# Performance work log

Measured on AMD Instinct MI355X. Metric: run time of the kernel, lower is better.

Reference implementation:

```python
import jax, jax.numpy as jnp
import numpy as np

CHUNK_SIZE = 1024  # module default chunk_size


def setup_inputs() -> dict:
    key = jax.random.key(0)
    kq, kk, kv = jax.random.split(key, 3)
    B, H, S, D = 2, 16, 2048, 64
    q = jax.random.normal(kq, (B, H, S, D), dtype=jnp.float32)
    k = jax.random.normal(kk, (B, H, S, D), dtype=jnp.float32)
    v = jax.random.normal(kv, (B, H, S, D), dtype=jnp.float32)
    return {"q": q, "k": k, "v": v}


def reference(q, k, v):
    # Chunked causal attention: q split into chunks of CHUNK_SIZE along seq,
    # each chunk attends to the full K/V with causal mask (tril, diagonal=start).
    B, H, S, D = q.shape
    scale = D ** (-0.5)
    cs = CHUNK_SIZE
    nc = S // cs  # S is a multiple of chunk_size here
    qc = q.reshape(B, H, nc, cs, D)
    # scores: [B, H, nc, cs, S]
    scores = jnp.einsum('bhncd,bhsd->bhncs', qc, k) * scale
    # causal mask per chunk: key position j visible iff j <= chunk_start + i
    row = (jnp.arange(nc) * cs)[:, None, None] + jnp.arange(cs)[None, :, None]  # [nc, cs, 1]
    col = jnp.arange(S)[None, None, :]  # [1, 1, S]
    causal = col <= row  # [nc, cs, S]
    scores = jnp.where(causal[None, None], scores, -jnp.inf)
    attn = jax.nn.softmax(scores, axis=-1)
    out = jnp.einsum('bhncs,bhsd->bhncd', attn, v)
    return out.reshape(B, H, S, D)
```

## Files before the change

kernel.cpp:

```cpp
#include <hip/hip_runtime.h>

typedef __bf16 bf16x8 __attribute__((ext_vector_type(8)));
typedef float f32x4 __attribute__((ext_vector_type(4)));

#define S_LEN 2048
#define D_DIM 64
#define NHEAD 32

typedef __attribute__((address_space(1))) const void gas;
typedef __attribute__((address_space(3))) void las;

__global__ __launch_bounds__(256) void convert_kv(const float* __restrict__ K,
                                                  const float* __restrict__ V,
                                                  __bf16* __restrict__ Kb,
                                                  __bf16* __restrict__ Vtg) {
    const int head = blockIdx.y;
    const int s0   = blockIdx.x * 64;
    const int tr   = threadIdx.x >> 2;
    const int tc   = (threadIdx.x & 3) << 4;
    const size_t ib = (size_t)head * (S_LEN * D_DIM) + (size_t)(s0 + tr) * D_DIM + tc;

    __shared__ __bf16 tb[64][72];

    {
        const float* kr = K + ib;
        f32x4 a = *(const f32x4*)kr, b = *(const f32x4*)(kr + 4),
              c = *(const f32x4*)(kr + 8), d = *(const f32x4*)(kr + 12);
        bf16x8 o0, o1;
        #pragma unroll
        for (int e = 0; e < 4; ++e) {
            o0[e] = (__bf16)a[e]; o0[e + 4] = (__bf16)b[e];
            o1[e] = (__bf16)c[e]; o1[e + 4] = (__bf16)d[e];
        }
        __bf16* ko = Kb + ib;
        *(bf16x8*)ko = o0; *(bf16x8*)(ko + 8) = o1;
    }
    {
        const float* vr = V + ib;
        f32x4 a = *(const f32x4*)vr, b = *(const f32x4*)(vr + 4),
              c = *(const f32x4*)(vr + 8), d = *(const f32x4*)(vr + 12);
        #pragma unroll
        for (int e = 0; e < 4; ++e) {
            tb[tc +  e][tr] = (__bf16)a[e];
            tb[tc + 4 + e][tr] = (__bf16)b[e];
            tb[tc + 8 + e][tr] = (__bf16)c[e];
            tb[tc + 12 + e][tr] = (__bf16)d[e];
        }
    }
    __syncthreads();
    {
        bf16x8 o0, o1;
        #pragma unroll
        for (int e = 0; e < 8; ++e) { o0[e] = tb[tr][tc + e]; o1[e] = tb[tr][tc + 8 + e]; }
        __bf16* vo = Vtg + (size_t)head * (D_DIM * S_LEN) + (size_t)tr * S_LEN + s0 + tc;
        *(bf16x8*)vo = o0; *(bf16x8*)(vo + 8) = o1;
    }
}

__global__ __launch_bounds__(256, 4) void attn_fwd(const float* __restrict__ Q,
                                                   const __bf16* __restrict__ Kb,
                                                   const __bf16* __restrict__ Vg,
                                                   float* __restrict__ O) {
    const int b    = blockIdx.x;
    const int xcd  = b & 7;
    const int cs   = (b >> 3) & 31;
    const int j    = b >> 8;
    const int head = xcd * 4 + (cs >> 3);
    const int slot = cs & 7;
    const int chunk = (j == 0) ? slot : (j == 1) ? (31 - slot)
                    : (j == 2) ? (slot + 8) : (23 - slot);

    const int tid  = threadIdx.x;
    const int wave = tid >> 6;
    const int lane = tid & 63;
    const int l15  = lane & 15;
    const int lhi  = lane >> 4;

    const int q0 = chunk * 64 + wave * 16;
    const size_t qbase = (size_t)head * (S_LEN * D_DIM);
    const size_t vbase = (size_t)head * (D_DIM * S_LEN);
    const float qscale = 0.125f * 1.44269504088896340736f;

    __shared__ __align__(16) __bf16 Klds[2][64][64];
    __shared__ __align__(16) __bf16 Vt[2][64][64];
    __shared__ __align__(16) __bf16 Plds[4][16][64];

    const int xsw = (lane & 7) ^ ((lane >> 3) & 7);
    const size_t kOff = (size_t)(lane >> 3) * D_DIM + (size_t)xsw * 8;
    const size_t vOff = (size_t)(lane >> 3) * S_LEN + (size_t)xsw * 8;
    const __bf16* kgw = Kb + qbase + (size_t)(wave * 16) * D_DIM + kOff;
    const __bf16* vgw = Vg + vbase + (size_t)(wave * 16) * S_LEN + vOff;

    bf16x8 qf[2];
    {
        const float* qrow = Q + qbase + (size_t)(q0 + l15) * D_DIM + lhi * 8;
        #pragma unroll
        for (int h = 0; h < 2; ++h) {
            f32x4 a = *(const f32x4*)(qrow + h * 32);
            f32x4 bq = *(const f32x4*)(qrow + h * 32 + 4);
            bf16x8 t;
            #pragma unroll
            for (int e = 0; e < 4; ++e) { t[e] = (__bf16)(a[e] * qscale); t[e + 4] = (__bf16)(bq[e] * qscale); }
            qf[h] = t;
        }
    }

    f32x4 acc[4];
    #pragma unroll
    for (int td = 0; td < 4; ++td) acc[td] = (f32x4){0.f, 0.f, 0.f, 0.f};
    float m_r = -1e30f, l_r = 0.f;

    auto stage = [&](int kv0, int bufi) {
        const __bf16* kg = kgw + (size_t)kv0 * D_DIM;
        const __bf16* vg = vgw + kv0;
        __builtin_amdgcn_global_load_lds((gas*)kg,                 (las*)&Klds[bufi][wave * 16][0],     16, 0, 0);
        __builtin_amdgcn_global_load_lds((gas*)(kg + 8 * D_DIM),   (las*)&Klds[bufi][wave * 16 + 8][0], 16, 0, 0);
        __builtin_amdgcn_global_load_lds((gas*)vg,                 (las*)&Vt[bufi][wave * 16][0],       16, 0, 0);
        __builtin_amdgcn_global_load_lds((gas*)(vg + 8 * S_LEN),   (las*)&Vt[bufi][wave * 16 + 8][0],   16, 0, 0);
    };

    stage(0, 0);

    const int nt = chunk + 1;
    for (int kt = 0; kt < nt; ++kt) {
        const int cur = kt & 1;
        asm volatile("s_waitcnt vmcnt(0)" ::: "memory");
        __syncthreads();

        if (kt + 1 < nt) stage((kt + 1) << 6, cur ^ 1);

        f32x4 s[4];
        #pragma unroll
        for (int ct = 0; ct < 4; ++ct) s[ct] = (f32x4){0.f, 0.f, 0.f, 0.f};
        __builtin_amdgcn_s_setprio(1);
        #pragma unroll
        for (int h = 0; h < 2; ++h) {
            #pragma unroll
            for (int ct = 0; ct < 4; ++ct) {
                const int krow = ct * 16 + l15;
                bf16x8 kf = *(const bf16x8*)&Klds[cur][krow][(h * 32 + lhi * 8) ^ ((l15 & 7) << 3)];
                s[ct] = __builtin_amdgcn_mfma_f32_16x16x32_bf16(kf, qf[h], s[ct], 0, 0, 0);
            }
        }
        __builtin_amdgcn_s_setprio(0);

        if (kt == nt - 1) {
            const int kv0 = kt << 6;
            const int qg = q0 + l15;
            #pragma unroll
            for (int ct = 0; ct < 4; ++ct)
                #pragma unroll
                for (int r = 0; r < 4; ++r) {
                    const int kg = kv0 + ct * 16 + lhi * 4 + r;
                    if (kg > qg) s[ct][r] = -1e30f;
                }
        }

        float mm = fmaxf(fmaxf(fmaxf(s[0][0], s[0][1]), fmaxf(s[0][2], s[0][3])),
                         fmaxf(fmaxf(s[1][0], s[1][1]), fmaxf(s[1][2], s[1][3])));
        mm = fmaxf(mm, fmaxf(fmaxf(fmaxf(s[2][0], s[2][1]), fmaxf(s[2][2], s[2][3])),
                             fmaxf(fmaxf(s[3][0], s[3][1]), fmaxf(s[3][2], s[3][3]))));
        mm = fmaxf(mm, __shfl_xor(mm, 16));
        mm = fmaxf(mm, __shfl_xor(mm, 32));
        if (!__all(mm - m_r <= 8.0f)) {
            const float mn = fmaxf(m_r, mm);
            const float f = exp2f(m_r - mn);
            m_r = mn;
            l_r *= f;
            #pragma unroll
            for (int r = 0; r < 4; ++r) {
                const float fr = __shfl(f, lhi * 4 + r);
                #pragma unroll
                for (int td = 0; td < 4; ++td) acc[td][r] *= fr;
            }
        }
        float ps = 0.f;
        #pragma unroll
        for (int ct = 0; ct < 4; ++ct)
            #pragma unroll
            for (int r = 0; r < 4; ++r) {
                const float p = exp2f(s[ct][r] - m_r);
                s[ct][r] = p;
                ps += p;
            }
        ps += __shfl_xor(ps, 16);
        ps += __shfl_xor(ps, 32);
        l_r += ps;

        #pragma unroll
        for (int ct = 0; ct < 4; ++ct) {
            union { __bf16 h[4]; unsigned long long u; } pw;
            #pragma unroll
            for (int r = 0; r < 4; ++r) pw.h[r] = (__bf16)s[ct][r];
            *(unsigned long long*)&Plds[wave][l15][(ct * 16 + lhi * 4) ^ ((l15 & 7) << 3)] = pw.u;
        }
        asm volatile("s_waitcnt lgkmcnt(0)" ::: "memory");
        bf16x8 pf[2];
        #pragma unroll
        for (int kh = 0; kh < 2; ++kh)
            pf[kh] = *(const bf16x8*)&Plds[wave][l15][(kh * 32 + lhi * 8) ^ ((l15 & 7) << 3)];
        asm volatile("" ::: "memory");

        __builtin_amdgcn_s_setprio(1);
        #pragma unroll
        for (int kh = 0; kh < 2; ++kh) {
            #pragma unroll
            for (int td = 0; td < 4; ++td) {
                const int vrow = td * 16 + l15;
                bf16x8 vf = *(const bf16x8*)&Vt[cur][vrow][(kh * 32 + lhi * 8) ^ ((vrow & 7) << 3)];
                acc[td] = __builtin_amdgcn_mfma_f32_16x16x32_bf16(pf[kh], vf, acc[td], 0, 0, 0);
            }
        }
        __builtin_amdgcn_s_setprio(0);
    }

    float* orow = O + qbase + (size_t)q0 * D_DIM;
    #pragma unroll
    for (int r = 0; r < 4; ++r) {
        const float inv = 1.0f / __shfl(l_r, lhi * 4 + r);
        #pragma unroll
        for (int td = 0; td < 4; ++td)
            orow[(size_t)(lhi * 4 + r) * D_DIM + td * 16 + l15] = acc[td][r] * inv;
    }
}

__global__ __launch_bounds__(256, 4) void attn_fwd_fb(const float* __restrict__ Q,
                                                      const float* __restrict__ K,
                                                      const float* __restrict__ V,
                                                      float* __restrict__ O) {
    const int b    = blockIdx.x;
    const int xcd  = b & 7;
    const int cs   = (b >> 3) & 31;
    const int j    = b >> 8;
    const int head = xcd * 4 + (cs >> 3);
    const int slot = cs & 7;
    const int chunk = (j == 0) ? slot : (j == 1) ? (31 - slot)
                    : (j == 2) ? (slot + 8) : (23 - slot);

    const int tid  = threadIdx.x;
    const int wave = tid >> 6;
    const int lane = tid & 63;
    const int l15  = lane & 15;
    const int lhi  = lane >> 4;

    const int q0 = chunk * 64 + wave * 16;
    const size_t base = (size_t)head * (S_LEN * D_DIM);
    const float qscale = 0.125f * 1.44269504088896340736f;

    __shared__ __align__(16) __bf16 Klds[2][64][64];
    __shared__ __align__(16) __bf16 Vt[2][64][64];
    __shared__ __align__(16) __bf16 Plds[4][16][64];

    const int rk = tid >> 2;
    const int ck = (tid & 3) << 4;
    const int kp = tid & 31;
    const int dc = tid >> 5;
    const int swk = (rk & 7) << 3;

    bf16x8 qf[2];
    {
        const float* qrow = Q + base + (size_t)(q0 + l15) * D_DIM + lhi * 8;
        #pragma unroll
        for (int h = 0; h < 2; ++h) {
            f32x4 a = *(const f32x4*)(qrow + h * 32);
            f32x4 bq = *(const f32x4*)(qrow + h * 32 + 4);
            bf16x8 t;
            #pragma unroll
            for (int e = 0; e < 4; ++e) { t[e] = (__bf16)(a[e] * qscale); t[e + 4] = (__bf16)(bq[e] * qscale); }
            qf[h] = t;
        }
    }

    f32x4 acc[4];
    #pragma unroll
    for (int td = 0; td < 4; ++td) acc[td] = (f32x4){0.f, 0.f, 0.f, 0.f};
    float m_r = -1e30f, l_r = 0.f;

    f32x4 pk[4], pva[2], pvb[2];
    {
        const float* ks = K + base + (size_t)rk * D_DIM + ck;
        #pragma unroll
        for (int i = 0; i < 4; ++i) pk[i] = *(const f32x4*)(ks + 4 * i);
        const float* v0 = V + base + (size_t)(2 * kp) * D_DIM + dc * 8;
        pva[0] = *(const f32x4*)v0;           pva[1] = *(const f32x4*)(v0 + 4);
        pvb[0] = *(const f32x4*)(v0 + D_DIM); pvb[1] = *(const f32x4*)(v0 + D_DIM + 4);
        bf16x8 k0, k1;
        #pragma unroll
        for (int e = 0; e < 4; ++e) {
            k0[e] = (__bf16)pk[0][e]; k0[e + 4] = (__bf16)pk[1][e];
            k1[e] = (__bf16)pk[2][e]; k1[e + 4] = (__bf16)pk[3][e];
        }
        *(bf16x8*)&Klds[0][rk][ck ^ swk] = k0;
        *(bf16x8*)&Klds[0][rk][(ck + 8) ^ swk] = k1;
        #pragma unroll
        for (int jj = 0; jj < 8; ++jj) {
            const int d = dc * 8 + jj;
            const float av = (jj < 4) ? pva[0][jj & 3] : pva[1][jj & 3];
            const float bv = (jj < 4) ? pvb[0][jj & 3] : pvb[1][jj & 3];
            union { __bf16 h[2]; unsigned int u; } t;
            t.h[0] = (__bf16)av; t.h[1] = (__bf16)bv;
            *(unsigned int*)&Vt[0][d][(2 * kp) ^ ((d & 7) << 3)] = t.u;
        }
    }

    const int nt = chunk + 1;
    for (int kt = 0; kt < nt; ++kt) {
        const int cur = kt & 1;
        __syncthreads();
        const bool pre = (kt + 1 < nt);
        if (pre) {
            const int kv1 = (kt + 1) << 6;
            const float* ks = K + base + (size_t)(kv1 + rk) * D_DIM + ck;
            #pragma unroll
            for (int i = 0; i < 4; ++i) pk[i] = *(const f32x4*)(ks + 4 * i);
            const float* v0 = V + base + (size_t)(kv1 + 2 * kp) * D_DIM + dc * 8;
            pva[0] = *(const f32x4*)v0;           pva[1] = *(const f32x4*)(v0 + 4);
            pvb[0] = *(const f32x4*)(v0 + D_DIM); pvb[1] = *(const f32x4*)(v0 + D_DIM + 4);
        }

        f32x4 s[4];
        #pragma unroll
        for (int ct = 0; ct < 4; ++ct) s[ct] = (f32x4){0.f, 0.f, 0.f, 0.f};
        #pragma unroll
        for (int h = 0; h < 2; ++h) {
            #pragma unroll
            for (int ct = 0; ct < 4; ++ct) {
                const int krow = ct * 16 + l15;
                bf16x8 kf = *(const bf16x8*)&Klds[cur][krow][(h * 32 + lhi * 8) ^ ((l15 & 7) << 3)];
                s[ct] = __builtin_amdgcn_mfma_f32_16x16x32_bf16(kf, qf[h], s[ct], 0, 0, 0);
            }
        }

        if (kt == nt - 1) {
            const int kv0 = kt << 6;
            const int qg = q0 + l15;
            #pragma unroll
            for (int ct = 0; ct < 4; ++ct)
                #pragma unroll
                for (int r = 0; r < 4; ++r) {
                    const int kg = kv0 + ct * 16 + lhi * 4 + r;
                    if (kg > qg) s[ct][r] = -1e30f;
                }
        }

        float mm = fmaxf(fmaxf(fmaxf(s[0][0], s[0][1]), fmaxf(s[0][2], s[0][3])),
                         fmaxf(fmaxf(s[1][0], s[1][1]), fmaxf(s[1][2], s[1][3])));
        mm = fmaxf(mm, fmaxf(fmaxf(fmaxf(s[2][0], s[2][1]), fmaxf(s[2][2], s[2][3])),
                             fmaxf(fmaxf(s[3][0], s[3][1]), fmaxf(s[3][2], s[3][3]))));
        mm = fmaxf(mm, __shfl_xor(mm, 16));
        mm = fmaxf(mm, __shfl_xor(mm, 32));
        if (!__all(mm - m_r <= 8.0f)) {
            const float mn = fmaxf(m_r, mm);
            const float f = exp2f(m_r - mn);
            m_r = mn;
            l_r *= f;
            #pragma unroll
            for (int r = 0; r < 4; ++r) {
                const float fr = __shfl(f, lhi * 4 + r);
                #pragma unroll
                for (int td = 0; td < 4; ++td) acc[td][r] *= fr;
            }
        }
        float ps = 0.f;
        #pragma unroll
        for (int ct = 0; ct < 4; ++ct)
            #pragma unroll
            for (int r = 0; r < 4; ++r) {
                const float p = exp2f(s[ct][r] - m_r);
                s[ct][r] = p;
                ps += p;
            }
        ps += __shfl_xor(ps, 16);
        ps += __shfl_xor(ps, 32);
        l_r += ps;

        #pragma unroll
        for (int ct = 0; ct < 4; ++ct) {
            union { __bf16 h[4]; unsigned long long u; } pw;
            #pragma unroll
            for (int r = 0; r < 4; ++r) pw.h[r] = (__bf16)s[ct][r];
            *(unsigned long long*)&Plds[wave][l15][(ct * 16 + lhi * 4) ^ ((l15 & 7) << 3)] = pw.u;
        }
        asm volatile("s_waitcnt lgkmcnt(0)" ::: "memory");
        bf16x8 pf[2];
        #pragma unroll
        for (int kh = 0; kh < 2; ++kh)
            pf[kh] = *(const bf16x8*)&Plds[wave][l15][(kh * 32 + lhi * 8) ^ ((l15 & 7) << 3)];
        asm volatile("" ::: "memory");

        #pragma unroll
        for (int kh = 0; kh < 2; ++kh) {
            #pragma unroll
            for (int td = 0; td < 4; ++td) {
                const int vrow = td * 16 + l15;
                bf16x8 vf = *(const bf16x8*)&Vt[cur][vrow][(kh * 32 + lhi * 8) ^ ((vrow & 7) << 3)];
                acc[td] = __builtin_amdgcn_mfma_f32_16x16x32_bf16(pf[kh], vf, acc[td], 0, 0, 0);
            }
        }

        if (pre) {
            const int nxt = cur ^ 1;
            bf16x8 k0, k1;
            #pragma unroll
            for (int e = 0; e < 4; ++e) {
                k0[e] = (__bf16)pk[0][e]; k0[e + 4] = (__bf16)pk[1][e];
                k1[e] = (__bf16)pk[2][e]; k1[e + 4] = (__bf16)pk[3][e];
            }
            *(bf16x8*)&Klds[nxt][rk][ck ^ swk] = k0;
            *(bf16x8*)&Klds[nxt][rk][(ck + 8) ^ swk] = k1;
            #pragma unroll
            for (int jj = 0; jj < 8; ++jj) {
                const int d = dc * 8 + jj;
                const float av = (jj < 4) ? pva[0][jj & 3] : pva[1][jj & 3];
                const float bv = (jj < 4) ? pvb[0][jj & 3] : pvb[1][jj & 3];
                union { __bf16 h[2]; unsigned int u; } t;
                t.h[0] = (__bf16)av; t.h[1] = (__bf16)bv;
                *(unsigned int*)&Vt[nxt][d][(2 * kp) ^ ((d & 7) << 3)] = t.u;
            }
        }
    }

    float* orow = O + base + (size_t)q0 * D_DIM;
    #pragma unroll
    for (int r = 0; r < 4; ++r) {
        const float inv = 1.0f / __shfl(l_r, lhi * 4 + r);
        #pragma unroll
        for (int td = 0; td < 4; ++td)
            orow[(size_t)(lhi * 4 + r) * D_DIM + td * 16 + l15] = acc[td][r] * inv;
    }
}

extern "C" void kernel_launch(void* const* d_in, const int* in_sizes, int n_in,
                              void* d_out, int out_size, void* d_ws, size_t ws_size,
                              hipStream_t stream) {
    const float* q = (const float*)d_in[0];
    const float* k = (const float*)d_in[1];
    const float* v = (const float*)d_in[2];
    float* o = (float*)d_out;
    const size_t elems = (size_t)NHEAD * S_LEN * D_DIM;
    if (ws_size >= 2 * elems * sizeof(__bf16)) {
        __bf16* Kb  = (__bf16*)d_ws;
        __bf16* Vtg = Kb + elems;
        convert_kv<<<dim3(32, 32), dim3(256), 0, stream>>>(k, v, Kb, Vtg);
        attn_fwd<<<dim3(1024), dim3(256), 0, stream>>>(q, Kb, Vtg, o);
    } else {
        attn_fwd_fb<<<dim3(1024), dim3(256), 0, stream>>>(q, k, v, o);
    }
}
```

Before: 62.21 us.

## Switch to 32x32 MFMA tiles with register-resident P and split-KV load balancing

```diff
diff --git a/kernel.cpp b/kernel.cpp
--- a/kernel.cpp
+++ b/kernel.cpp
@@ -2,13 +2,27 @@
 
 typedef __bf16 bf16x8 __attribute__((ext_vector_type(8)));
 typedef float f32x4 __attribute__((ext_vector_type(4)));
+typedef float f32x16 __attribute__((ext_vector_type(16)));
 
 #define S_LEN 2048
 #define D_DIM 64
 #define NHEAD 32
+#define PART_FLOATS 8448
 
 typedef __attribute__((address_space(1))) const void gas;
 typedef __attribute__((address_space(3))) void las;
+
+#define J(c, t0, nt) ((unsigned short)((c) | ((t0) << 4) | ((nt) << 9)))
+__device__ const unsigned short TRIP[24] = {
+    J(15,0,16), J(15,16,16), J(0,0,2),
+    J(7,0,16),  J(13,0,14),  J(1,0,4),
+    J(14,0,15), J(12,0,13),  J(2,0,6),
+    J(14,15,15),J(10,0,11),  J(3,0,8),
+    J(13,14,14),J(10,11,11), J(8,0,9),
+    J(6,0,14),  J(9,0,10),   J(9,10,10),
+    J(12,13,13),J(11,0,12),  J(8,9,9),
+    J(11,12,12),J(5,0,12),   J(4,0,10),
+};
 
 __global__ __launch_bounds__(256) void convert_kv(const float* __restrict__ K,
                                                   const float* __restrict__ V,
@@ -57,33 +71,35 @@
     }
 }
 
-__global__ __launch_bounds__(256, 4) void attn_fwd(const float* __restrict__ Q,
-                                                   const __bf16* __restrict__ Kb,
-                                                   const __bf16* __restrict__ Vg,
-                                                   float* __restrict__ O) {
+__global__ __launch_bounds__(256, 3) void attn32(const float* __restrict__ Q,
+                                                 const __bf16* __restrict__ Kb,
+                                                 const __bf16* __restrict__ Vg,
+                                                 float* __restrict__ O,
+                                                 float* __restrict__ Pp) {
     const int b    = blockIdx.x;
     const int xcd  = b & 7;
-    const int cs   = (b >> 3) & 31;
-    const int j    = b >> 8;
-    const int head = xcd * 4 + (cs >> 3);
-    const int slot = cs & 7;
-    const int chunk = (j == 0) ? slot : (j == 1) ? (31 - slot)
-                    : (j == 2) ? (slot + 8) : (23 - slot);
+    const int cu   = (b >> 3) & 31;
+    const int pass = b >> 8;
+    const int head = xcd * 4 + (cu >> 3);
+    const unsigned short jw = TRIP[(cu & 7) * 3 + pass];
+    const int chunk = jw & 15;
+    const int t0    = (jw >> 4) & 31;
+    const int nt    = jw >> 9;
 
     const int tid  = threadIdx.x;
     const int wave = tid >> 6;
     const int lane = tid & 63;
-    const int l15  = lane & 15;
-    const int lhi  = lane >> 4;
-
-    const int q0 = chunk * 64 + wave * 16;
+    const int l31  = lane & 31;
+    const int hi   = lane >> 5;
+    const int sw31 = (l31 & 7) << 3;
+
+    const int q0w = chunk * 128 + wave * 32;
     const size_t qbase = (size_t)head * (S_LEN * D_DIM);
     const size_t vbase = (size_t)head * (D_DIM * S_LEN);
     const float qscale = 0.125f * 1.44269504088896340736f;
 
     __shared__ __align__(16) __bf16 Klds[2][64][64];
     __shared__ __align__(16) __bf16 Vt[2][64][64];
-    __shared__ __align__(16) __bf16 Plds[4][16][64];
 
     const int xsw = (lane & 7) ^ ((lane >> 3) & 7);
     const size_t kOff = (size_t)(lane >> 3) * D_DIM + (size_t)xsw * 8;
@@ -91,136 +107,196 @@
     const __bf16* kgw = Kb + qbase + (size_t)(wave * 16) * D_DIM + kOff;
     const __bf16* vgw = Vg + vbase + (size_t)(wave * 16) * S_LEN + vOff;
 
-    bf16x8 qf[2];
+    bf16x8 qf[4];
     {
-        const float* qrow = Q + qbase + (size_t)(q0 + l15) * D_DIM + lhi * 8;
-        #pragma unroll
-        for (int h = 0; h < 2; ++h) {
-            f32x4 a = *(const f32x4*)(qrow + h * 32);
-            f32x4 bq = *(const f32x4*)(qrow + h * 32 + 4);
+        const float* qrow = Q + qbase + (size_t)(q0w + l31) * D_DIM + hi * 8;
+        #pragma unroll
+        for (int kd = 0; kd < 4; ++kd) {
+            f32x4 a = *(const f32x4*)(qrow + kd * 16);
+            f32x4 c = *(const f32x4*)(qrow + kd * 16 + 4);
             bf16x8 t;
             #pragma unroll
-            for (int e = 0; e < 4; ++e) { t[e] = (__bf16)(a[e] * qscale); t[e + 4] = (__bf16)(bq[e] * qscale); }
-            qf[h] = t;
-        }
-    }
-
-    f32x4 acc[4];
+            for (int e = 0; e < 4; ++e) { t[e] = (__bf16)(a[e] * qscale); t[e + 4] = (__bf16)(c[e] * qscale); }
+            qf[kd] = t;
+        }
+    }
+
+    f32x16 acc0 = {0.f}, acc1 = {0.f};
     #pragma unroll
-    for (int td = 0; td < 4; ++td) acc[td] = (f32x4){0.f, 0.f, 0.f, 0.f};
+    for (int r = 0; r < 16; ++r) { acc0[r] = 0.f; acc1[r] = 0.f; }
     float m_r = -1e30f, l_r = 0.f;
 
     auto stage = [&](int kv0, int bufi) {
         const __bf16* kg = kgw + (size_t)kv0 * D_DIM;
         const __bf16* vg = vgw + kv0;
-        __builtin_amdgcn_global_load_lds((gas*)kg,                 (las*)&Klds[bufi][wave * 16][0],     16, 0, 0);
-        __builtin_amdgcn_global_load_lds((gas*)(kg + 8 * D_DIM),   (las*)&Klds[bufi][wave * 16 + 8][0], 16, 0, 0);
-        __builtin_amdgcn_global_load_lds((gas*)vg,                 (las*)&Vt[bufi][wave * 16][0],       16, 0, 0);
-        __builtin_amdgcn_global_load_lds((gas*)(vg + 8 * S_LEN),   (las*)&Vt[bufi][wave * 16 + 8][0],   16, 0, 0);
+        __builtin_amdgcn_global_load_lds((gas*)kg,               (las*)&Klds[bufi][wave * 16][0],     16, 0, 0);
+        __builtin_amdgcn_global_load_lds((gas*)(kg + 8 * D_DIM), (las*)&Klds[bufi][wave * 16 + 8][0], 16, 0, 0);
+        __builtin_amdgcn_global_load_lds((gas*)vg,               (las*)&Vt[bufi][wave * 16][0],       16, 0, 0);
+        __builtin_amdgcn_global_load_lds((gas*)(vg + 8 * S_LEN), (las*)&Vt[bufi][wave * 16 + 8][0],   16, 0, 0);
     };
-
-    stage(0, 0);
-
-    const int nt = chunk + 1;
-    for (int kt = 0; kt < nt; ++kt) {
-        const int cur = kt & 1;
+    auto cvtpk = [](float lo, float hh) {
+        unsigned int r;
+        asm("v_cvt_pk_bf16_f32 %0, %1, %2" : "=v"(r) : "v"(lo), "v"(hh));
+        return r;
+    };
+
+    stage(t0 << 6, 0);
+
+    for (int it = 0; it < nt; ++it) {
+        const int cur = it & 1;
         asm volatile("s_waitcnt vmcnt(0)" ::: "memory");
         __syncthreads();
 
-        if (kt + 1 < nt) stage((kt + 1) << 6, cur ^ 1);
-
-        f32x4 s[4];
-        #pragma unroll
-        for (int ct = 0; ct < 4; ++ct) s[ct] = (f32x4){0.f, 0.f, 0.f, 0.f};
-        __builtin_amdgcn_s_setprio(1);
-        #pragma unroll
-        for (int h = 0; h < 2; ++h) {
-            #pragma unroll
-            for (int ct = 0; ct < 4; ++ct) {
-                const int krow = ct * 16 + l15;
-                bf16x8 kf = *(const bf16x8*)&Klds[cur][krow][(h * 32 + lhi * 8) ^ ((l15 & 7) << 3)];
-                s[ct] = __builtin_amdgcn_mfma_f32_16x16x32_bf16(kf, qf[h], s[ct], 0, 0, 0);
-            }
-        }
-        __builtin_amdgcn_s_setprio(0);
-
-        if (kt == nt - 1) {
-            const int kv0 = kt << 6;
-            const int qg = q0 + l15;
-            #pragma unroll
-            for (int ct = 0; ct < 4; ++ct)
+        if (it + 1 < nt) stage((t0 + it + 1) << 6, cur ^ 1);
+        const int kv0 = (t0 + it) << 6;
+
+        if (kv0 <= q0w + 31) {
+            f32x16 s0, s1;
+            #pragma unroll
+            for (int r = 0; r < 16; ++r) { s0[r] = 0.f; s1[r] = 0.f; }
+            __builtin_amdgcn_s_setprio(1);
+            #pragma unroll
+            for (int kd = 0; kd < 4; ++kd) {
+                bf16x8 kf0 = *(const bf16x8*)&Klds[cur][l31][(kd * 16 + hi * 8) ^ sw31];
+                bf16x8 kf1 = *(const bf16x8*)&Klds[cur][32 + l31][(kd * 16 + hi * 8) ^ sw31];
+                s0 = __builtin_amdgcn_mfma_f32_32x32x16_bf16(kf0, qf[kd], s0, 0, 0, 0);
+                s1 = __builtin_amdgcn_mfma_f32_32x32x16_bf16(kf1, qf[kd], s1, 0, 0, 0);
+            }
+            __builtin_amdgcn_s_setprio(0);
+
+            if (kv0 + 63 > q0w) {
+                const int qg = q0w + l31;
                 #pragma unroll
-                for (int r = 0; r < 4; ++r) {
-                    const int kg = kv0 + ct * 16 + lhi * 4 + r;
-                    if (kg > qg) s[ct][r] = -1e30f;
+                for (int r = 0; r < 16; ++r) {
+                    const int cr = (r & 3) + 8 * (r >> 2) + 4 * hi;
+                    if (kv0 + cr > qg)      s0[r] = -1e30f;
+                    if (kv0 + 32 + cr > qg) s1[r] = -1e30f;
                 }
-        }
-
-        float mm = fmaxf(fmaxf(fmaxf(s[0][0], s[0][1]), fmaxf(s[0][2], s[0][3])),
-                         fmaxf(fmaxf(s[1][0], s[1][1]), fmaxf(s[1][2], s[1][3])));
-        mm = fmaxf(mm, fmaxf(fmaxf(fmaxf(s[2][0], s[2][1]), fmaxf(s[2][2], s[2][3])),
-                             fmaxf(fmaxf(s[3][0], s[3][1]), fmaxf(s[3][2], s[3][3]))));
-        mm = fmaxf(mm, __shfl_xor(mm, 16));
-        mm = fmaxf(mm, __shfl_xor(mm, 32));
-        if (!__all(mm - m_r <= 8.0f)) {
-            const float mn = fmaxf(m_r, mm);
-            const float f = exp2f(m_r - mn);
-            m_r = mn;
-            l_r *= f;
-            #pragma unroll
-            for (int r = 0; r < 4; ++r) {
-                const float fr = __shfl(f, lhi * 4 + r);
+            }
+
+            float mm = -1e30f;
+            #pragma unroll
+            for (int r = 0; r < 16; ++r) mm = fmaxf(mm, fmaxf(s0[r], s1[r]));
+            mm = fmaxf(mm, __shfl_xor(mm, 32));
+            if (!__all(mm - m_r <= 8.0f)) {
+                const float mn = fmaxf(m_r, mm);
+                const float f = exp2f(m_r - mn);
+                m_r = mn;
+                l_r *= f;
                 #pragma unroll
-                for (int td = 0; td < 4; ++td) acc[td][r] *= fr;
-            }
-        }
-        float ps = 0.f;
-        #pragma unroll
-        for (int ct = 0; ct < 4; ++ct)
-            #pragma unroll
-            for (int r = 0; r < 4; ++r) {
-                const float p = exp2f(s[ct][r] - m_r);
-                s[ct][r] = p;
-                ps += p;
-            }
-        ps += __shfl_xor(ps, 16);
-        ps += __shfl_xor(ps, 32);
-        l_r += ps;
-
-        #pragma unroll
-        for (int ct = 0; ct < 4; ++ct) {
-            union { __bf16 h[4]; unsigned long long u; } pw;
-            #pragma unroll
-            for (int r = 0; r < 4; ++r) pw.h[r] = (__bf16)s[ct][r];
-            *(unsigned long long*)&Plds[wave][l15][(ct * 16 + lhi * 4) ^ ((l15 & 7) << 3)] = pw.u;
-        }
-        asm volatile("s_waitcnt lgkmcnt(0)" ::: "memory");
-        bf16x8 pf[2];
-        #pragma unroll
-        for (int kh = 0; kh < 2; ++kh)
-            pf[kh] = *(const bf16x8*)&Plds[wave][l15][(kh * 32 + lhi * 8) ^ ((l15 & 7) << 3)];
-        asm volatile("" ::: "memory");
-
-        __builtin_amdgcn_s_setprio(1);
-        #pragma unroll
-        for (int kh = 0; kh < 2; ++kh) {
-            #pragma unroll
-            for (int td = 0; td < 4; ++td) {
-                const int vrow = td * 16 + l15;
-                bf16x8 vf = *(const bf16x8*)&Vt[cur][vrow][(kh * 32 + lhi * 8) ^ ((vrow & 7) << 3)];
-                acc[td] = __builtin_amdgcn_mfma_f32_16x16x32_bf16(pf[kh], vf, acc[td], 0, 0, 0);
-            }
-        }
-        __builtin_amdgcn_s_setprio(0);
-    }
-
-    float* orow = O + qbase + (size_t)q0 * D_DIM;
+                for (int r = 0; r < 16; ++r) {
+                    const float fr = __shfl(f, (r & 3) + 8 * (r >> 2) + 4 * hi);
+                    acc0[r] *= fr; acc1[r] *= fr;
+                }
+            }
+            float ps = 0.f, ps2 = 0.f;
+            #pragma unroll
+            for (int r = 0; r < 16; ++r) {
+                s0[r] = exp2f(s0[r] - m_r); ps  += s0[r];
+                s1[r] = exp2f(s1[r] - m_r); ps2 += s1[r];
+            }
+            ps += ps2;
+            ps += __shfl_xor(ps, 32);
+            l_r += ps;
+
+            __builtin_amdgcn_s_setprio(1);
+            {
+                unsigned int w01 = cvtpk(s0[0],  s0[1]),  w23 = cvtpk(s0[2],  s0[3]);
+                unsigned int w45 = cvtpk(s0[4],  s0[5]),  w67 = cvtpk(s0[6],  s0[7]);
+                unsigned int w89 = cvtpk(s0[8],  s0[9]),  wab = cvtpk(s0[10], s0[11]);
+                unsigned int wcd = cvtpk(s0[12], s0[13]), wef = cvtpk(s0[14], s0[15]);
+                asm("v_permlane32_swap_b32 %0, %1" : "+v"(w01), "+v"(w45));
+                asm("v_permlane32_swap_b32 %0, %1" : "+v"(w23), "+v"(w67));
+                asm("v_permlane32_swap_b32 %0, %1" : "+v"(w89), "+v"(wcd));
+                asm("v_permlane32_swap_b32 %0, %1" : "+v"(wab), "+v"(wef));
+                union { unsigned int u[4]; bf16x8 v; } f0 = {{w01, w23, w45, w67}};
+                union { unsigned int u[4]; bf16x8 v; } f1 = {{w89, wab, wcd, wef}};
+                bf16x8 v00 = *(const bf16x8*)&Vt[cur][l31][(hi * 8) ^ sw31];
+                bf16x8 v01 = *(const bf16x8*)&Vt[cur][32 + l31][(hi * 8) ^ sw31];
+                acc0 = __builtin_amdgcn_mfma_f32_32x32x16_bf16(f0.v, v00, acc0, 0, 0, 0);
+                acc1 = __builtin_amdgcn_mfma_f32_32x32x16_bf16(f0.v, v01, acc1, 0, 0, 0);
+                bf16x8 v10 = *(const bf16x8*)&Vt[cur][l31][(16 + hi * 8) ^ sw31];
+                bf16x8 v11 = *(const bf16x8*)&Vt[cur][32 + l31][(16 + hi * 8) ^ sw31];
+                acc0 = __builtin_amdgcn_mfma_f32_32x32x16_bf16(f1.v, v10, acc0, 0, 0, 0);
+                acc1 = __builtin_amdgcn_mfma_f32_32x32x16_bf16(f1.v, v11, acc1, 0, 0, 0);
+            }
+            {
+                unsigned int w01 = cvtpk(s1[0],  s1[1]),  w23 = cvtpk(s1[2],  s1[3]);
+                unsigned int w45 = cvtpk(s1[4],  s1[5]),  w67 = cvtpk(s1[6],  s1[7]);
+                unsigned int w89 = cvtpk(s1[8],  s1[9]),  wab = cvtpk(s1[10], s1[11]);
+                unsigned int wcd = cvtpk(s1[12], s1[13]), wef = cvtpk(s1[14], s1[15]);
+                asm("v_permlane32_swap_b32 %0, %1" : "+v"(w01), "+v"(w45));
+                asm("v_permlane32_swap_b32 %0, %1" : "+v"(w23), "+v"(w67));
+                asm("v_permlane32_swap_b32 %0, %1" : "+v"(w89), "+v"(wcd));
+                asm("v_permlane32_swap_b32 %0, %1" : "+v"(wab), "+v"(wef));
+                union { unsigned int u[4]; bf16x8 v; } f2 = {{w01, w23, w45, w67}};
+                union { unsigned int u[4]; bf16x8 v; } f3 = {{w89, wab, wcd, wef}};
+                bf16x8 v20 = *(const bf16x8*)&Vt[cur][l31][(32 + hi * 8) ^ sw31];
+                bf16x8 v21 = *(const bf16x8*)&Vt[cur][32 + l31][(32 + hi * 8) ^ sw31];
+                acc0 = __builtin_amdgcn_mfma_f32_32x32x16_bf16(f2.v, v20, acc0, 0, 0, 0);
+                acc1 = __builtin_amdgcn_mfma_f32_32x32x16_bf16(f2.v, v21, acc1, 0, 0, 0);
+                bf16x8 v30 = *(const bf16x8*)&Vt[cur][l31][(48 + hi * 8) ^ sw31];
+                bf16x8 v31 = *(const bf16x8*)&Vt[cur][32 + l31][(48 + hi * 8) ^ sw31];
+                acc0 = __builtin_amdgcn_mfma_f32_32x32x16_bf16(f3.v, v30, acc0, 0, 0, 0);
+                acc1 = __builtin_amdgcn_mfma_f32_32x32x16_bf16(f3.v, v31, acc1, 0, 0, 0);
+            }
+            __builtin_amdgcn_s_setprio(0);
+        }
+    }
+
+    if (chunk < 8) {
+        const float inv_own = 1.0f / l_r;
+        float* ob = O + qbase + (size_t)(chunk * 128 + wave * 32) * D_DIM + l31;
+        #pragma unroll
+        for (int r = 0; r < 16; ++r) {
+            const int cr = (r & 3) + 8 * (r >> 2) + 4 * hi;
+            const float inv = __shfl(inv_own, cr);
+            ob[(size_t)cr * D_DIM]      = acc0[r] * inv;
+            ob[(size_t)cr * D_DIM + 32] = acc1[r] * inv;
+        }
+    } else {
+        const int seg = (t0 != 0) ? 1 : 0;
+        float* pp = Pp + (size_t)((head * 8 + (chunk - 8)) * 2 + seg) * PART_FLOATS;
+        if (hi == 0) {
+            pp[wave * 32 + l31] = m_r;
+            pp[128 + wave * 32 + l31] = l_r;
+        }
+        float* pb = pp + 256 + (size_t)(wave * 32) * 64 + l31;
+        #pragma unroll
+        for (int r = 0; r < 16; ++r) {
+            const int cr = (r & 3) + 8 * (r >> 2) + 4 * hi;
+            pb[(size_t)cr * 64]      = acc0[r];
+            pb[(size_t)cr * 64 + 32] = acc1[r];
+        }
+    }
+}
+
+__global__ __launch_bounds__(256) void combine(const float* __restrict__ Pp,
+                                               float* __restrict__ O) {
+    const int head = blockIdx.y;
+    const int ch   = blockIdx.x;
+    const float* PA = Pp + (size_t)((head * 8 + ch) * 2) * PART_FLOATS;
+    const float* PB = PA + PART_FLOATS;
+    const int row = threadIdx.x >> 1;
+    const int c0  = (threadIdx.x & 1) << 5;
+
+    const float mA = PA[row], lA = PA[128 + row];
+    const float mB = PB[row], lB = PB[128 + row];
+    const float M  = fmaxf(mA, mB);
+    const float wA = exp2f(mA - M), wB = exp2f(mB - M);
+    const float inv = 1.0f / (lA * wA + lB * wB);
+
+    const float* a = PA + 256 + (size_t)row * 64 + c0;
+    const float* b = PB + 256 + (size_t)row * 64 + c0;
+    float* o = O + (size_t)head * (S_LEN * D_DIM) + (size_t)((8 + ch) * 128 + row) * D_DIM + c0;
     #pragma unroll
-    for (int r = 0; r < 4; ++r) {
-        const float inv = 1.0f / __shfl(l_r, lhi * 4 + r);
-        #pragma unroll
-        for (int td = 0; td < 4; ++td)
-            orow[(size_t)(lhi * 4 + r) * D_DIM + td * 16 + l15] = acc[td][r] * inv;
+    for (int i = 0; i < 8; ++i) {
+        f32x4 va = *(const f32x4*)(a + 4 * i);
+        f32x4 vb = *(const f32x4*)(b + 4 * i);
+        f32x4 vo;
+        #pragma unroll
+        for (int e = 0; e < 4; ++e) vo[e] = (va[e] * wA + vb[e] * wB) * inv;
+        *(f32x4*)(o + 4 * i) = vo;
     }
 }
 
@@ -438,11 +514,15 @@
     const float* v = (const float*)d_in[2];
     float* o = (float*)d_out;
     const size_t elems = (size_t)NHEAD * S_LEN * D_DIM;
-    if (ws_size >= 2 * elems * sizeof(__bf16)) {
+    const size_t kvBytes = 2 * elems * sizeof(__bf16);
+    const size_t partBytes = (size_t)512 * PART_FLOATS * sizeof(float);
+    if (ws_size >= kvBytes + partBytes) {
         __bf16* Kb  = (__bf16*)d_ws;
         __bf16* Vtg = Kb + elems;
+        float* Pp   = (float*)((char*)d_ws + kvBytes);
         convert_kv<<<dim3(32, 32), dim3(256), 0, stream>>>(k, v, Kb, Vtg);
-        attn_fwd<<<dim3(1024), dim3(256), 0, stream>>>(q, Kb, Vtg, o);
+        attn32<<<dim3(768), dim3(256), 0, stream>>>(q, Kb, Vtg, o, Pp);
+        combine<<<dim3(8, 32), dim3(256), 0, stream>>>(Pp, o);
     } else {
         attn_fwd_fb<<<dim3(1024), dim3(256), 0, stream>>>(q, k, v, o);
     }
```

After: 62.68 us. No clear change (+0.8%).
